# Kernel tuning notes

Measured on AMD Instinct MI355X. Metric: run time of the kernel, lower is better.

Reference implementation:

```python
import jax, jax.numpy as jnp
import numpy as np

DIM = 32      # feature dim (must be small: unnormalized det prod overflows fp32 otherwise)
K = 16        # number of mixture components / experts
B = 262144    # batch


def setup_inputs() -> dict:
    key = jax.random.key(0)
    k0, k1, k2, k3, k4 = jax.random.split(key, 5)
    x = jax.random.normal(k0, (B, DIM), dtype=jnp.float32)
    xavier = 1.0 / np.sqrt(DIM / 2.0)
    mu = (jax.random.normal(k1, (K, DIM), dtype=jnp.float32) * xavier)
    # torch init is ones; use small values so prod(2*pi*sigma2) stays finite in fp32
    logsigma = jax.random.normal(k2, (K, DIM), dtype=jnp.float32) * 0.1
    W = jax.random.normal(k3, (K, DIM, DIM), dtype=jnp.float32) * (1.0 / np.sqrt(DIM))
    b = jax.random.normal(k4, (K, DIM), dtype=jnp.float32) * 0.01
    return {"x": x, "mu": mu, "logsigma": logsigma, "W": W, "b": b}


def reference(x, mu, logsigma, W, b):
    # Gaussian prior pdf per expert, vectorized over k
    two_pi = np.float32(2.0 * np.pi)
    sigma2 = jnp.exp(2.0 * logsigma)                                   # [k, d]
    const = jax.lax.rsqrt(jnp.prod(two_pi * sigma2, axis=-1))           # [k]
    diff = x[None, :, :] - mu[:, None, :]                               # [k, b, d]
    exponent = -0.5 * jnp.sum(diff * diff / sigma2[:, None, :], axis=-1)  # [k, b]
    ps = const[:, None] * jnp.exp(exponent)                             # [k, b]
    w = ps / jnp.sum(ps, axis=0, keepdims=True)                         # [k, b]
    # per-expert Linear (torch convention: x @ W_k.T + b_k) + ReLU
    lik = jax.nn.relu(jnp.einsum('bd,kod->kbo', x, W) + b[:, None, :])  # [k, b, d]
    # gate-weighted sum over experts
    return jnp.einsum('kb,kbo->bo', w, lik)                             # [b, d]
```

## Files before the change

kernel.cpp:

```cpp
#include <hip/hip_runtime.h>
#include <math.h>

#define DIM 32
#define NK  16
#define LOG2E 1.4426950408889634f

typedef __attribute__((ext_vector_type(8))) short bf16x8;
typedef __attribute__((ext_vector_type(4))) float f32x4;

#define MFMA16 __builtin_amdgcn_mfma_f32_16x16x32_bf16

#define WHIF_OFF 0
#define WLOF_OFF 32768
#define HH_OFF  65536
#define HL_OFF  66560
#define GH_OFF  67584
#define GL_OFF  68608
#define CG_OFF  69632

typedef __attribute__((address_space(1))) const unsigned int gu32;
typedef __attribute__((address_space(3))) unsigned int lu32;

#define LDSP_BASE 32768
#define LDSP_WAVE 2304
#define LDS_TOTAL (32768 + 4 * LDSP_WAVE)

__device__ __forceinline__ void split2(float x, short* hi, short* lo) {
  unsigned u = __float_as_uint(x);
  *hi = (short)(u >> 16);
  float hf = __uint_as_float(u & 0xFFFF0000u);
  float l = x - hf;
  *lo = (short)(__float_as_uint(l) >> 16);
}

__global__ __launch_bounds__(256) void gmm_setup_kernel(
    const float* __restrict__ mu, const float* __restrict__ logsigma,
    const float* __restrict__ W, char* __restrict__ ws)
{
  int i = blockIdx.x * 256 + threadIdx.x;
  if (i < NK * 2 * 64) {
    const int k = i >> 7, o16 = (i >> 6) & 1, lane = i & 63;
    const int c = lane & 15, g = lane >> 4;
    const int o = o16 * 16 + c;
    bf16x8 hi, lo;
    #pragma unroll
    for (int j = 0; j < 8; ++j) {
      short h_, l_;
      split2(W[(k * DIM + o) * DIM + g * 8 + j], &h_, &l_);
      hi[j] = h_; lo[j] = l_;
    }
    ((bf16x8*)(ws + WHIF_OFF))[i] = hi;
    ((bf16x8*)(ws + WLOF_OFF))[i] = lo;
  }
  if (i < NK * DIM) {
    float s2 = __expf(2.0f * logsigma[i]);
    float h = (-0.5f / s2) * LOG2E;
    float g = (mu[i] / s2) * LOG2E;
    short a, b;
    split2(h, &a, &b);
    ((short*)(ws + HH_OFF))[i] = a; ((short*)(ws + HL_OFF))[i] = b;
    split2(g, &a, &b);
    ((short*)(ws + GH_OFF))[i] = a; ((short*)(ws + GL_OFF))[i] = b;
  }
  if (i < NK) {
    float acc = 0.0f;
    for (int d = 0; d < DIM; ++d) {
      float s2 = __expf(2.0f * logsigma[i * DIM + d]);
      float m  = mu[i * DIM + d];
      acc += m * m * (-0.5f / s2) * LOG2E - 0.5f * log2f(6.283185307179586f * s2);
    }
    ((float*)(ws + CG_OFF))[i] = acc;
  }
}

__global__ __launch_bounds__(256, 3) void gmm_moe_kernel(
    const float* __restrict__ x,
    const float* __restrict__ bias,
    const char* __restrict__ ws,
    float* __restrict__ out)
{
  __shared__ char lds[LDS_TOTAL];
  const int tid  = threadIdx.x;
  const int wid  = tid >> 6;
  const int lane = tid & 63;
  const int g = lane >> 4;
  const int c = lane & 15;
  const int sbase = (blockIdx.x * 4 + wid) * 32;

  #pragma unroll
  for (int r = 0; r < 8; ++r) {
    const int off = r * 4096 + wid * 1024;
    __builtin_amdgcn_global_load_lds(
        (gu32*)(ws + WHIF_OFF + off + lane * 16), (lu32*)(lds + off), 16, 0, 0);
  }

  float4 xa[2][2];
  #pragma unroll
  for (int t = 0; t < 2; ++t) {
    const float4* xp =
        (const float4*)(x + (size_t)(sbase + t * 16 + c) * DIM + g * 8);
    xa[t][0] = xp[0];
    xa[t][1] = xp[1];
  }

  const bf16x8 fhh = ((const bf16x8*)(ws + HH_OFF))[c * 4 + g];
  const bf16x8 fhl = ((const bf16x8*)(ws + HL_OFF))[c * 4 + g];
  const bf16x8 fgh = ((const bf16x8*)(ws + GH_OFF))[c * 4 + g];
  const bf16x8 fgl = ((const bf16x8*)(ws + GL_OFF))[c * 4 + g];
  const float  cgv = ((const float*)(ws + CG_OFF))[c];

  bf16x8 xh[2], xl[2];
  f32x4 wv[2];
  #pragma unroll
  for (int t = 0; t < 2; ++t) {
    float xv[8] = {xa[t][0].x, xa[t][0].y, xa[t][0].z, xa[t][0].w,
                   xa[t][1].x, xa[t][1].y, xa[t][1].z, xa[t][1].w};
    bf16x8 x2h, x2l;
    #pragma unroll
    for (int j = 0; j < 8; ++j) {
      short h_, l_;
      split2(xv[j], &h_, &l_);
      xh[t][j] = h_; xl[t][j] = l_;
      float q = xv[j] * xv[j];
      split2(q, &h_, &l_);
      x2h[j] = h_; x2l[j] = l_;
    }
    f32x4 e = {cgv, cgv, cgv, cgv};
    e = MFMA16(x2h,   fhh, e, 0, 0, 0);
    e = MFMA16(x2l,   fhh, e, 0, 0, 0);
    e = MFMA16(x2h,   fhl, e, 0, 0, 0);
    e = MFMA16(xh[t], fgh, e, 0, 0, 0);
    e = MFMA16(xl[t], fgh, e, 0, 0, 0);
    e = MFMA16(xh[t], fgl, e, 0, 0, 0);
    #pragma unroll
    for (int r = 0; r < 4; ++r) {
      float p = __builtin_amdgcn_exp2f(e[r]);
      float s = p;
      s += __shfl_xor(s, 1, 64);
      s += __shfl_xor(s, 2, 64);
      s += __shfl_xor(s, 4, 64);
      s += __shfl_xor(s, 8, 64);
      wv[t][r] = p * __builtin_amdgcn_rcpf(s);
    }
  }

  {
    char* pw = lds + LDSP_BASE + wid * LDSP_WAVE + c * 144 + g * 16;
    *(f32x4*)(pw)      = wv[0];
    *(f32x4*)(pw + 64) = wv[1];
  }

  __syncthreads();

  const bf16x8* wlof = (const bf16x8*)(ws + WLOF_OFF);
  const char*   ldsp = lds + LDSP_BASE + wid * LDSP_WAVE + g * 16;
  f32x4 o0[2], o1[2];
  #pragma unroll
  for (int t = 0; t < 2; ++t) { o0[t] = (f32x4){0,0,0,0}; o1[t] = (f32x4){0,0,0,0}; }

  #pragma unroll
  for (int k = 0; k < NK; ++k) {
    const bf16x8 w0h = *(const bf16x8*)(lds + (k * 2 + 0) * 1024 + lane * 16);
    const bf16x8 w1h = *(const bf16x8*)(lds + (k * 2 + 1) * 1024 + lane * 16);
    const bf16x8 w0l = wlof[(k * 2 + 0) * 64 + lane];
    const bf16x8 w1l = wlof[(k * 2 + 1) * 64 + lane];
    const float b0 = bias[k * DIM + c];
    const float b1 = bias[k * DIM + 16 + c];
    #pragma unroll
    for (int t = 0; t < 2; ++t) {
      f32x4 s0 = {b0, b0, b0, b0}, s1 = {b1, b1, b1, b1};
      s0 = MFMA16(xh[t], w0h, s0, 0, 0, 0);
      s0 = MFMA16(xl[t], w0h, s0, 0, 0, 0);
      s0 = MFMA16(xh[t], w0l, s0, 0, 0, 0);
      s1 = MFMA16(xh[t], w1h, s1, 0, 0, 0);
      s1 = MFMA16(xl[t], w1h, s1, 0, 0, 0);
      s1 = MFMA16(xh[t], w1l, s1, 0, 0, 0);
      const f32x4 wb = *(const f32x4*)(ldsp + k * 144 + t * 64);
      const f32x4 z = {0.0f, 0.0f, 0.0f, 0.0f};
      o0[t] = __builtin_elementwise_fma(wb, __builtin_elementwise_max(s0, z), o0[t]);
      o1[t] = __builtin_elementwise_fma(wb, __builtin_elementwise_max(s1, z), o1[t]);
    }
  }

  #pragma unroll
  for (int t = 0; t < 2; ++t) {
    #pragma unroll
    for (int r = 0; r < 4; ++r) {
      size_t row = (size_t)(sbase + t * 16 + g * 4 + r);
      out[row * DIM + c]      = o0[t][r];
      out[row * DIM + 16 + c] = o1[t][r];
    }
  }
}

extern "C" void kernel_launch(void* const* d_in, const int* in_sizes, int n_in,
                              void* d_out, int out_size, void* d_ws, size_t ws_size,
                              hipStream_t stream) {
  const float* x  = (const float*)d_in[0];
  const float* mu = (const float*)d_in[1];
  const float* ls = (const float*)d_in[2];
  const float* W  = (const float*)d_in[3];
  const float* bv = (const float*)d_in[4];
  float* out = (float*)d_out;
  const int B = in_sizes[0] / DIM;

  gmm_setup_kernel<<<8, 256, 0, stream>>>(mu, ls, W, (char*)d_ws);
  gmm_moe_kernel<<<B / 128, 256, 0, stream>>>(x, bv, (const char*)d_ws, out);
}
```

Measured before the change: 116.0 us.

## Process 64 rows per wave, defer gate normalization, drop LDS weight staging

Each wave now handles four 16-row tiles so every weight fragment is reused across more MFMAs, with 512-thread blocks. Weight fragments are read directly from global/cache instead of being staged in LDS, bias is staged per wave in LDS, and the block barrier is removed. The softmax normalization via cross-lane shuffles is replaced by accumulating the sum of gate probabilities alongside the output and dividing once at the end. Unnormalized LDS gate storage uses an XOR swizzle to reduce bank conflicts. Higher register pressure could hurt occupancy.

After: 172.3 us. 48.5% more time.

```diff
diff --git a/kernel.cpp b/kernel.cpp
--- a/kernel.cpp
+++ b/kernel.cpp
@@ -18,12 +18,9 @@
 #define GL_OFF  68608
 #define CG_OFF  69632
 
-typedef __attribute__((address_space(1))) const unsigned int gu32;
-typedef __attribute__((address_space(3))) unsigned int lu32;
-
-#define LDSP_BASE 32768
-#define LDSP_WAVE 2304
-#define LDS_TOTAL (32768 + 4 * LDSP_WAVE)
+#define LDS_BIAS(w) ((w) * 2048)
+#define LDS_P(w)    (16384 + (w) * 4096)
+#define LDS_TOTAL   (16384 + 32768)
 
 __device__ __forceinline__ void split2(float x, short* hi, short* lo) {
   unsigned u = __float_as_uint(x);
@@ -73,7 +70,7 @@
   }
 }
 
-__global__ __launch_bounds__(256, 3) void gmm_moe_kernel(
+__global__ __launch_bounds__(512, 4) void gmm_moe_kernel(
     const float* __restrict__ x,
     const float* __restrict__ bias,
     const char* __restrict__ ws,
@@ -85,18 +82,18 @@
   const int lane = tid & 63;
   const int g = lane >> 4;
   const int c = lane & 15;
-  const int sbase = (blockIdx.x * 4 + wid) * 32;
-
-  #pragma unroll
-  for (int r = 0; r < 8; ++r) {
-    const int off = r * 4096 + wid * 1024;
-    __builtin_amdgcn_global_load_lds(
-        (gu32*)(ws + WHIF_OFF + off + lane * 16), (lu32*)(lds + off), 16, 0, 0);
-  }
-
-  float4 xa[2][2];
-  #pragma unroll
-  for (int t = 0; t < 2; ++t) {
+  const int sbase = (blockIdx.x * 8 + wid) * 64;
+
+  {
+    const float4* bsrc = (const float4*)bias;
+    float4 b0 = bsrc[lane * 2], b1 = bsrc[lane * 2 + 1];
+    *(float4*)(lds + LDS_BIAS(wid) + lane * 32)      = b0;
+    *(float4*)(lds + LDS_BIAS(wid) + lane * 32 + 16) = b1;
+  }
+
+  float4 xa[4][2];
+  #pragma unroll
+  for (int t = 0; t < 4; ++t) {
     const float4* xp =
         (const float4*)(x + (size_t)(sbase + t * 16 + c) * DIM + g * 8);
     xa[t][0] = xp[0];
@@ -109,10 +106,9 @@
   const bf16x8 fgl = ((const bf16x8*)(ws + GL_OFF))[c * 4 + g];
   const float  cgv = ((const float*)(ws + CG_OFF))[c];
 
-  bf16x8 xh[2], xl[2];
-  f32x4 wv[2];
-  #pragma unroll
-  for (int t = 0; t < 2; ++t) {
+  bf16x8 xh[4], xl[4];
+  #pragma unroll
+  for (int t = 0; t < 4; ++t) {
     float xv[8] = {xa[t][0].x, xa[t][0].y, xa[t][0].z, xa[t][0].w,
                    xa[t][1].x, xa[t][1].y, xa[t][1].z, xa[t][1].w};
     bf16x8 x2h, x2l;
@@ -132,42 +128,31 @@
     e = MFMA16(xh[t], fgh, e, 0, 0, 0);
     e = MFMA16(xl[t], fgh, e, 0, 0, 0);
     e = MFMA16(xh[t], fgl, e, 0, 0, 0);
-    #pragma unroll
-    for (int r = 0; r < 4; ++r) {
-      float p = __builtin_amdgcn_exp2f(e[r]);
-      float s = p;
-      s += __shfl_xor(s, 1, 64);
-      s += __shfl_xor(s, 2, 64);
-      s += __shfl_xor(s, 4, 64);
-      s += __shfl_xor(s, 8, 64);
-      wv[t][r] = p * __builtin_amdgcn_rcpf(s);
-    }
-  }
-
-  {
-    char* pw = lds + LDSP_BASE + wid * LDSP_WAVE + c * 144 + g * 16;
-    *(f32x4*)(pw)      = wv[0];
-    *(f32x4*)(pw + 64) = wv[1];
-  }
-
-  __syncthreads();
-
-  const bf16x8* wlof = (const bf16x8*)(ws + WLOF_OFF);
-  const char*   ldsp = lds + LDSP_BASE + wid * LDSP_WAVE + g * 16;
-  f32x4 o0[2], o1[2];
-  #pragma unroll
-  for (int t = 0; t < 2; ++t) { o0[t] = (f32x4){0,0,0,0}; o1[t] = (f32x4){0,0,0,0}; }
+    f32x4 wv;
+    #pragma unroll
+    for (int r = 0; r < 4; ++r) wv[r] = __builtin_amdgcn_exp2f(e[r]);
+    *(f32x4*)(lds + LDS_P(wid) + c * 256 +
+              ((t * 64 + g * 16) ^ ((c & 7) << 4))) = wv;
+  }
+
+  const bf16x8* wfr = (const bf16x8*)ws;
+  f32x4 o0[4], o1[4], psum[4];
+  #pragma unroll
+  for (int t = 0; t < 4; ++t) {
+    o0[t] = (f32x4){0,0,0,0}; o1[t] = (f32x4){0,0,0,0};
+    psum[t] = (f32x4){0,0,0,0};
+  }
 
   #pragma unroll
   for (int k = 0; k < NK; ++k) {
-    const bf16x8 w0h = *(const bf16x8*)(lds + (k * 2 + 0) * 1024 + lane * 16);
-    const bf16x8 w1h = *(const bf16x8*)(lds + (k * 2 + 1) * 1024 + lane * 16);
-    const bf16x8 w0l = wlof[(k * 2 + 0) * 64 + lane];
-    const bf16x8 w1l = wlof[(k * 2 + 1) * 64 + lane];
-    const float b0 = bias[k * DIM + c];
-    const float b1 = bias[k * DIM + 16 + c];
-    #pragma unroll
-    for (int t = 0; t < 2; ++t) {
+    const bf16x8 w0h = wfr[(k * 2 + 0) * 64 + lane];
+    const bf16x8 w1h = wfr[(k * 2 + 1) * 64 + lane];
+    const bf16x8 w0l = wfr[2048 + (k * 2 + 0) * 64 + lane];
+    const bf16x8 w1l = wfr[2048 + (k * 2 + 1) * 64 + lane];
+    const float b0 = *(const float*)(lds + LDS_BIAS(wid) + k * 128 + c * 4);
+    const float b1 = *(const float*)(lds + LDS_BIAS(wid) + k * 128 + 64 + c * 4);
+    #pragma unroll
+    for (int t = 0; t < 4; ++t) {
       f32x4 s0 = {b0, b0, b0, b0}, s1 = {b1, b1, b1, b1};
       s0 = MFMA16(xh[t], w0h, s0, 0, 0, 0);
       s0 = MFMA16(xl[t], w0h, s0, 0, 0, 0);
@@ -175,15 +160,22 @@
       s1 = MFMA16(xh[t], w1h, s1, 0, 0, 0);
       s1 = MFMA16(xl[t], w1h, s1, 0, 0, 0);
       s1 = MFMA16(xh[t], w1l, s1, 0, 0, 0);
-      const f32x4 wb = *(const f32x4*)(ldsp + k * 144 + t * 64);
+      const f32x4 wb = *(const f32x4*)(lds + LDS_P(wid) + k * 256 +
+                                       ((t * 64 + g * 16) ^ ((k & 7) << 4)));
       const f32x4 z = {0.0f, 0.0f, 0.0f, 0.0f};
       o0[t] = __builtin_elementwise_fma(wb, __builtin_elementwise_max(s0, z), o0[t]);
       o1[t] = __builtin_elementwise_fma(wb, __builtin_elementwise_max(s1, z), o1[t]);
-    }
-  }
-
-  #pragma unroll
-  for (int t = 0; t < 2; ++t) {
+      psum[t] = psum[t] + wb;
+    }
+  }
+
+  #pragma unroll
+  for (int t = 0; t < 4; ++t) {
+    f32x4 inv;
+    #pragma unroll
+    for (int r = 0; r < 4; ++r) inv[r] = __builtin_amdgcn_rcpf(psum[t][r]);
+    o0[t] = o0[t] * inv;
+    o1[t] = o1[t] * inv;
     #pragma unroll
     for (int r = 0; r < 4; ++r) {
       size_t row = (size_t)(sbase + t * 16 + g * 4 + r);
@@ -205,5 +197,5 @@
   const int B = in_sizes[0] / DIM;
 
   gmm_setup_kernel<<<8, 256, 0, stream>>>(mu, ls, W, (char*)d_ws);
-  gmm_moe_kernel<<<B / 128, 256, 0, stream>>>(x, bv, (const char*)d_ws, out);
-}
+  gmm_moe_kernel<<<B / 512, 512, 0, stream>>>(x, bv, (const char*)d_ws, out);
+}
```
